# Optimization experiments

Hardware: AMD Instinct MI355X
Metric: run time of the kernel (lower is better)

## Reference

```python
import jax, jax.numpy as jnp
import numpy as np

N, D = 16384, 32            # nodes, max neighbors (0-padded)
INP, U = 256, 128           # input_units, units
R, ENT = 8, 8               # relations, entity types (relation/entity id 0 = padding for relations)


def setup_inputs() -> dict:
    key = jax.random.key(0)
    ks = jax.random.split(key, 12)
    s = 0.05  # scale learned params for numerical sanity (torch init is raw randn)
    return {
        "node_state": jax.random.normal(ks[0], (N, INP), dtype=jnp.float32),
        "adjacency": jax.random.randint(ks[1], (N, D), 0, N + 1, dtype=jnp.int32),  # 0 = pad row
        "point_enc": jax.random.randint(ks[2], (N,), 0, ENT, dtype=jnp.int32),
        "relation_enc": jax.random.randint(ks[3], (N, D), 0, R, dtype=jnp.int32),   # 0 = pad edge
        "point_enc_w": jax.random.normal(ks[4], (ENT, INP, U), dtype=jnp.float32) * s,
        "relation_enc_w": jax.random.normal(ks[5], (R, U, U), dtype=jnp.float32) * s,
        "q_w": jax.random.normal(ks[6], (U, U), dtype=jnp.float32) * s,
        "k_w": jax.random.normal(ks[7], (U, U), dtype=jnp.float32) * s,
        "v_w": jax.random.normal(ks[8], (U, U), dtype=jnp.float32) * s,
        "fc_w": jax.random.normal(ks[9], (U, U), dtype=jnp.float32) * s,
        "fc_b": jax.random.normal(ks[10], (U,), dtype=jnp.float32) * s,
    }


def reference(node_state, adjacency, point_enc, relation_enc,
              point_enc_w, relation_enc_w, q_w, k_w, v_w, fc_w, fc_b):
    ent, inp, u = point_enc_w.shape
    r_cnt = relation_enc_w.shape[0]
    dt = node_state.dtype

    # center = node_state @ point_enc_w[point_enc]; loop over small fixed entity set
    # to avoid materializing an (N, INP, U) gathered weight tensor.
    center = jnp.zeros((node_state.shape[0], u), dtype=dt)
    for e in range(ent):
        center = center + jnp.where(point_enc[:, None] == e,
                                    node_state @ point_enc_w[e], 0.0)

    # prepend zero row: adjacency index 0 == padding neighbor
    padded = jnp.concatenate([jnp.zeros((1, u), dtype=dt), center], axis=0)  # (N+1, U)
    x = padded[adjacency]  # (N, D, U) gathered neighbor embeddings

    # neighbors = x @ relation_enc_w[relation_enc]; per-relation GEMM + mask
    # (same math as the per-edge gathered matmul, without the E*U*U blowup)
    neighbors = jnp.zeros_like(x)
    for r in range(r_cnt):
        neighbors = neighbors + jnp.where(relation_enc[..., None] == r,
                                          jnp.einsum('ndu,uv->ndv', x, relation_enc_w[r]), 0.0)

    scale = u ** 0.5
    q = (center @ q_w) / scale                               # (N, U)
    k = jnp.einsum('ndu,uv->ndv', neighbors, k_w) / scale    # (N, D, U)
    v = jnp.einsum('ndu,uv->ndv', neighbors, v_w)            # (N, D, U)

    scores = jnp.einsum('nu,ndu->nd', q, k)                  # (N, D)
    scores = jnp.where(relation_enc == 0, jnp.asarray(-1e9, dt), scores)
    attn = jax.nn.softmax(scores, axis=-1)                   # over neighbors
    agg = jnp.einsum('nd,ndu->nu', attn, v)                  # (N, U)

    return center + jax.nn.relu(agg @ fc_w + fc_b)           # (N, U)
```

## Files before the change

kernel.cpp:

```cpp
#include <hip/hip_runtime.h>

#define NNODE 16384
#define DD 32
#define INPC 256
#define UC 128
#define RC 8
#define EC 8

typedef __attribute__((ext_vector_type(8))) short short8;
typedef __attribute__((ext_vector_type(4))) float float4v;
typedef __attribute__((ext_vector_type(4))) unsigned uint4v;

__device__ __forceinline__ unsigned short f2bf(float f) {
    unsigned u = __builtin_bit_cast(unsigned, f);
    unsigned r = (u + 0x7FFFu + ((u >> 16) & 1u)) >> 16;
    return (unsigned short)r;
}
__device__ __forceinline__ float bf2f(unsigned short s) { return __builtin_bit_cast(float, (unsigned)s << 16); }

template <int CTRL>
__device__ __forceinline__ float dppq(float x) {
    return __builtin_bit_cast(float,
        __builtin_amdgcn_mov_dpp(__builtin_bit_cast(int, x), CTRL, 0xF, 0xF, true));
}
#define DPP_XOR1 0xB1
#define DPP_XOR2 0x4E

__device__ __forceinline__ short8 ld8bf(const float* p) {
    float4 v0 = *(const float4*)p;
    float4 v1 = *(const float4*)(p + 4);
    short8 a;
    a[0] = (short)f2bf(v0.x); a[1] = (short)f2bf(v0.y);
    a[2] = (short)f2bf(v0.z); a[3] = (short)f2bf(v0.w);
    a[4] = (short)f2bf(v1.x); a[5] = (short)f2bf(v1.y);
    a[6] = (short)f2bf(v1.z); a[7] = (short)f2bf(v1.w);
    return a;
}

__device__ __forceinline__ int bfrag_idx(int k, int col, int nct) {
    int ks = k >> 5, ct = col >> 4;
    int l = (((k >> 3) & 3) << 4) | (col & 15);
    return (((ks * nct + ct) << 6) + l) * 8 + (k & 7);
}

__global__ void k_setup(const float* __restrict__ pew, const float* __restrict__ qw,
                        const float* __restrict__ kw, const float* __restrict__ relw,
                        const float* __restrict__ vw, const float* __restrict__ fcw,
                        unsigned short* __restrict__ pewfrag,
                        unsigned short* __restrict__ BallQfrag, unsigned short* __restrict__ RVFfrag) {
    __shared__ unsigned short stage_s[128 * 132];
    __shared__ unsigned short mat_s[16 * 136];
    int b = blockIdx.x;
    if (b < 256) {
        #pragma unroll
        for (int it = 0; it < 4; ++it) {
            int id = it * 65536 + b * 256 + threadIdx.x;
            int e = id >> 15, k = (id >> 7) & 255, col = id & 127;
            pewfrag[(e << 15) + bfrag_idx(k, col, 8)] = f2bf(pew[id]);
        }
        return;
    }
    {
        int pb = b - 256;
        int r = pb & 7, i0 = (pb >> 3) * 16;
        int w = threadIdx.x >> 6, l = threadIdx.x & 63;
        int mrow = l & 15, kgrp = (l >> 4) << 3;
        const float* R = relw + r * (UC * UC);

        float4v accP[2] = {};
        #pragma unroll
        for (int ks = 0; ks < 4; ++ks) {
            short8 a = ld8bf(&qw[(i0 + mrow) * UC + ks * 32 + kgrp]);
            #pragma unroll
            for (int ci = 0; ci < 2; ++ci) {
                int ct = w * 2 + ci;
                short8 bf = ld8bf(&kw[(ct * 16 + mrow) * UC + ks * 32 + kgrp]);
                accP[ci] = __builtin_amdgcn_mfma_f32_16x16x32_bf16(a, bf, accP[ci], 0, 0, 0);
            }
        }
        #pragma unroll
        for (int ci = 0; ci < 2; ++ci)
            #pragma unroll
            for (int reg = 0; reg < 4; ++reg) {
                int row = ((l >> 4) << 2) + reg;
                int col = (w * 2 + ci) * 16 + mrow;
                mat_s[row * 136 + col] = f2bf(accP[ci][reg] * (1.0f / 128.0f));
            }
        for (int it = 0; it < 16; ++it) {
            int idx = it * 256 + threadIdx.x;
            int row = idx >> 5, col = (idx & 31) * 4;
            float4 v = *(const float4*)&vw[row * UC + col];
            uint2 o;
            o.x = (unsigned)f2bf(v.x) | ((unsigned)f2bf(v.y) << 16);
            o.y = (unsigned)f2bf(v.z) | ((unsigned)f2bf(v.w) << 16);
            *(uint2*)&stage_s[row * 132 + col] = o;
        }
        __syncthreads();

        float4v accM[2] = {}, accV[2] = {};
        #pragma unroll
        for (int ks = 0; ks < 4; ++ks) {
            short8 aM = *(const short8*)&mat_s[mrow * 136 + ks * 32 + kgrp];
            short8 aV = ld8bf(&R[(i0 + mrow) * UC + ks * 32 + kgrp]);
            #pragma unroll
            for (int ci = 0; ci < 2; ++ci) {
                int ct = w * 2 + ci;
                short8 bM = ld8bf(&R[(ct * 16 + mrow) * UC + ks * 32 + kgrp]);
                accM[ci] = __builtin_amdgcn_mfma_f32_16x16x32_bf16(aM, bM, accM[ci], 0, 0, 0);
                uint4v pv;
                #pragma unroll
                for (int jp = 0; jp < 4; ++jp) {
                    unsigned e0 = stage_s[(ks * 32 + kgrp + jp * 2) * 132 + ct * 16 + mrow];
                    unsigned e1 = stage_s[(ks * 32 + kgrp + jp * 2 + 1) * 132 + ct * 16 + mrow];
                    pv[jp] = e0 | (e1 << 16);
                }
                accV[ci] = __builtin_amdgcn_mfma_f32_16x16x32_bf16(
                    aV, __builtin_bit_cast(short8, pv), accV[ci], 0, 0, 0);
            }
        }
        #pragma unroll
        for (int ci = 0; ci < 2; ++ci)
            #pragma unroll
            for (int reg = 0; reg < 4; ++reg) {
                int i = i0 + ((l >> 4) << 2) + reg;
                int col = r * 128 + (w * 2 + ci) * 16 + mrow;
                BallQfrag[bfrag_idx(i, col, 64)] = f2bf(accM[ci][reg]);
            }
        __syncthreads();
        #pragma unroll
        for (int ci = 0; ci < 2; ++ci)
            #pragma unroll
            for (int reg = 0; reg < 4; ++reg)
                mat_s[(((l >> 4) << 2) + reg) * 136 + (w * 2 + ci) * 16 + mrow] = f2bf(accV[ci][reg]);
        for (int it = 0; it < 16; ++it) {
            int idx = it * 256 + threadIdx.x;
            int row = idx >> 5, col = (idx & 31) * 4;
            float4 v = *(const float4*)&fcw[row * UC + col];
            uint2 o;
            o.x = (unsigned)f2bf(v.x) | ((unsigned)f2bf(v.y) << 16);
            o.y = (unsigned)f2bf(v.z) | ((unsigned)f2bf(v.w) << 16);
            *(uint2*)&stage_s[row * 132 + col] = o;
        }
        __syncthreads();

        float4v accF[2] = {};
        #pragma unroll
        for (int ks = 0; ks < 4; ++ks) {
            short8 aF = *(const short8*)&mat_s[mrow * 136 + ks * 32 + kgrp];
            #pragma unroll
            for (int ci = 0; ci < 2; ++ci) {
                int ct = w * 2 + ci;
                uint4v pv;
                #pragma unroll
                for (int jp = 0; jp < 4; ++jp) {
                    unsigned e0 = stage_s[(ks * 32 + kgrp + jp * 2) * 132 + ct * 16 + mrow];
                    unsigned e1 = stage_s[(ks * 32 + kgrp + jp * 2 + 1) * 132 + ct * 16 + mrow];
                    pv[jp] = e0 | (e1 << 16);
                }
                accF[ci] = __builtin_amdgcn_mfma_f32_16x16x32_bf16(
                    aF, __builtin_bit_cast(short8, pv), accF[ci], 0, 0, 0);
            }
        }
        #pragma unroll
        for (int ci = 0; ci < 2; ++ci)
            #pragma unroll
            for (int reg = 0; reg < 4; ++reg) {
                int i = i0 + ((l >> 4) << 2) + reg;
                int col = (w * 2 + ci) * 16 + mrow;
                RVFfrag[bfrag_idx(r * 128 + i, col, 8)] = f2bf(accF[ci][reg]);
            }
    }
}

__global__ __launch_bounds__(256, 4)
void k_center(const float* __restrict__ ns, const unsigned short* __restrict__ pewfrag,
              const int* __restrict__ pe, unsigned short* __restrict__ center_bf) {
    int w = threadIdx.x >> 6, l = threadIdx.x & 63;
    int n0 = blockIdx.x * 16;
    int row = n0 + (l & 15);
    int ent = pe[row];

    short8 a[8];
    #pragma unroll
    for (int ks = 0; ks < 8; ++ks)
        a[ks] = ld8bf(&ns[(size_t)row * 256 + ks * 32 + ((l >> 4) << 3)]);

    float4v acc[2] = {};
    short8 z = {};
    for (int e = 0; e < 8; ++e) {
        if (!__any(ent == e)) continue;
        const unsigned short* pf = pewfrag + ((size_t)e << 15);
        #pragma unroll
        for (int ks = 0; ks < 8; ++ks) {
            short8 am = (ent == e) ? a[ks] : z;
            #pragma unroll
            for (int ci = 0; ci < 2; ++ci) {
                int ct = w * 2 + ci;
                short8 b = *(const short8*)&pf[(((ks * 8 + ct) << 6) + l) * 8];
                acc[ci] = __builtin_amdgcn_mfma_f32_16x16x32_bf16(am, b, acc[ci], 0, 0, 0);
            }
        }
    }
    #pragma unroll
    for (int reg = 0; reg < 4; ++reg) {
        int orow = n0 + ((l >> 4) << 2) + reg;
        #pragma unroll
        for (int ci = 0; ci < 2; ++ci)
            center_bf[(size_t)orow * 128 + (w * 2 + ci) * 16 + (l & 15)] = f2bf(acc[ci][reg]);
    }
}

#define QSTRIDE 1096
__global__ __launch_bounds__(256, 4)
void k_final(const unsigned short* __restrict__ center_bf,
             const unsigned short* __restrict__ BallQfrag,
             const unsigned short* __restrict__ RVFfrag,
             const int* __restrict__ adj, const int* __restrict__ rel,
             const float* __restrict__ fcb, float* __restrict__ out) {
    __shared__ unsigned short qlds[16 * QSTRIDE];
    int w = threadIdx.x >> 6, l = threadIdx.x & 63;
    int n0 = blockIdx.x * 16;

    int pk[4][2];
    #pragma unroll
    for (int q = 0; q < 4; ++q) {
        int n = n0 + w * 4 + q;
        #pragma unroll
        for (int t = 0; t < 2; ++t) {
            int ai = adj[n * DD + t * 16 + (l & 15)];
            int rv = rel[n * DD + t * 16 + (l & 15)];
            int rr = ai > 0 ? ai - 1 : 0;
            pk[q][t] = (rr << 5) | (rv << 1) | (ai != 0 ? 1 : 0);
        }
    }

    short8 xp[2][4];
    #pragma unroll
    for (int t = 0; t < 2; ++t)
        #pragma unroll
        for (int ks = 0; ks < 4; ++ks)
            xp[t][ks] = *(const short8*)&center_bf[(size_t)(pk[0][t] >> 5) * 128
                                                   + ks * 32 + ((l >> 4) << 3)];

    {
        short8 a[4];
        #pragma unroll
        for (int ks = 0; ks < 4; ++ks)
            a[ks] = *(const short8*)&center_bf[(size_t)(n0 + (l & 15)) * 128 + ks * 32 + ((l >> 4) << 3)];
        for (int ci = 0; ci < 16; ++ci) {
            int ct = w * 16 + ci;
            float4v acc = {};
            #pragma unroll
            for (int ks = 0; ks < 4; ++ks) {
                short8 b = *(const short8*)&BallQfrag[(((ks * 64 + ct) << 6) + l) * 8];
                acc = __builtin_amdgcn_mfma_f32_16x16x32_bf16(a[ks], b, acc, 0, 0, 0);
            }
            int r = ct >> 3;
            int ch = (ct & 7) * 16 + (l & 15);
            #pragma unroll
            for (int reg = 0; reg < 4; ++reg) {
                int rn = ((l >> 4) << 2) + reg;
                qlds[rn * QSTRIDE + r * 136 + ch] = f2bf(acc[reg]);
            }
        }
    }
    __syncthreads();

    #pragma unroll
    for (int q = 0; q < 4; ++q) {
        int tn = w * 4 + q;
        int p0 = pk[q][0], p1 = pk[q][1];
        int rv0 = (p0 >> 1) & 7, rv1 = (p1 >> 1) & 7;
        int va0 = p0 & 1, va1 = p1 & 1;

        float4v sc[2] = {};
        #pragma unroll
        for (int ks = 0; ks < 4; ++ks) {
            short8 qb = *(const short8*)&qlds[tn * QSTRIDE + (l & 7) * 136 + ks * 32 + ((l >> 4) << 3)];
            sc[0] = __builtin_amdgcn_mfma_f32_16x16x32_bf16(qb, xp[0][ks], sc[0], 0, 0, 0);
            sc[1] = __builtin_amdgcn_mfma_f32_16x16x32_bf16(qb, xp[1][ks], sc[1], 0, 0, 0);
        }

        int rsel = (l & 32) ? (p1 >> 5) : (p0 >> 5);
        int rows[8];
        #pragma unroll
        for (int jj = 0; jj < 8; ++jj)
            rows[jj] = __shfl(rsel, (l & 48) | (((l >> 4) & 1) * 8 + jj), 64);
        unsigned short g0[4][8];
        #pragma unroll
        for (int ct = 0; ct < 4; ++ct)
            #pragma unroll
            for (int jj = 0; jj < 8; ++jj)
                g0[ct][jj] = center_bf[(size_t)rows[jj] * 128 + ct * 16 + (l & 15)];

        if (q < 3) {
            #pragma unroll
            for (int t = 0; t < 2; ++t)
                #pragma unroll
                for (int ks = 0; ks < 4; ++ks)
                    xp[t][ks] = *(const short8*)&center_bf[(size_t)(pk[q + 1][t] >> 5) * 128
                                                           + ks * 32 + ((l >> 4) << 3)];
        }

        float sel0, sel1;
        {
            int r = rv0;
            float v01 = (r & 1) ? sc[0][1] : sc[0][0];
            float v23 = (r & 1) ? sc[0][3] : sc[0][2];
            float regv = (r & 2) ? v23 : v01;
            float s = __shfl(regv, ((r >> 2) << 4) | (l & 15), 64);
            if (!va0) s = 0.f;
            if (r == 0) s = -1e9f;
            sel0 = fminf(s, 60.f);
        }
        {
            int r = rv1;
            float v01 = (r & 1) ? sc[1][1] : sc[1][0];
            float v23 = (r & 1) ? sc[1][3] : sc[1][2];
            float regv = (r & 2) ? v23 : v01;
            float s = __shfl(regv, ((r >> 2) << 4) | (l & 15), 64);
            if (!va1) s = 0.f;
            if (r == 0) s = -1e9f;
            sel1 = fminf(s, 60.f);
        }

        float at0 = __expf(sel0);
        float at1 = __expf(sel1);
        float sm = at0 + at1;
        sm += dppq<DPP_XOR1>(sm);
        sm += dppq<DPP_XOR2>(sm);
        sm += __shfl_xor(sm, 4, 64);
        sm += __shfl_xor(sm, 8, 64);
        float inv = 1.0f / fmaxf(sm, 1e-30f);
        at0 *= inv; at1 *= inv;
        if (!va0) at0 = 0.f;
        if (!va1) at1 = 0.f;

        unsigned md0 = (unsigned)f2bf(at0) | ((unsigned)rv0 << 16);
        unsigned md1 = (unsigned)f2bf(at1) | ((unsigned)rv1 << 16);
        unsigned mdsel = (l >= 32) ? md1 : md0;
        unsigned aw[4];
        #pragma unroll
        for (int jp = 0; jp < 4; ++jp) {
            unsigned m0 = __shfl(mdsel, (l & 48) | (((l >> 4) & 1) * 8 + jp * 2), 64);
            unsigned m1 = __shfl(mdsel, (l & 48) | (((l >> 4) & 1) * 8 + jp * 2 + 1), 64);
            unsigned s0 = ((m0 >> 16) == (unsigned)(l & 15)) ? (m0 & 0xFFFFu) : 0u;
            unsigned s1 = ((m1 >> 16) == (unsigned)(l & 15)) ? (m1 & 0xFFFFu) : 0u;
            aw[jp] = s0 | (s1 << 16);
        }
        uint4v av = {aw[0], aw[1], aw[2], aw[3]};
        short8 afrag = __builtin_bit_cast(short8, av);

        #pragma unroll
        for (int ct = 0; ct < 4; ++ct) {
            uint4v bv = {(unsigned)g0[ct][0] | ((unsigned)g0[ct][1] << 16),
                         (unsigned)g0[ct][2] | ((unsigned)g0[ct][3] << 16),
                         (unsigned)g0[ct][4] | ((unsigned)g0[ct][5] << 16),
                         (unsigned)g0[ct][6] | ((unsigned)g0[ct][7] << 16)};
            float4v zc = {};
            float4v acc = __builtin_amdgcn_mfma_f32_16x16x32_bf16(
                afrag, __builtin_bit_cast(short8, bv), zc, 0, 0, 0);
            if (l < 32) {
                int rbase = (l >> 4) << 2;
                #pragma unroll
                for (int reg = 0; reg < 4; ++reg)
                    qlds[tn * QSTRIDE + (rbase + reg) * 136 + ct * 16 + (l & 15)] = f2bf(acc[reg]);
            }
        }

        unsigned short g1[4][8];
        #pragma unroll
        for (int c2 = 0; c2 < 4; ++c2)
            #pragma unroll
            for (int jj = 0; jj < 8; ++jj)
                g1[c2][jj] = center_bf[(size_t)rows[jj] * 128 + (c2 + 4) * 16 + (l & 15)];
        #pragma unroll
        for (int c2 = 0; c2 < 4; ++c2) {
            int ct = c2 + 4;
            uint4v bv = {(unsigned)g1[c2][0] | ((unsigned)g1[c2][1] << 16),
                         (unsigned)g1[c2][2] | ((unsigned)g1[c2][3] << 16),
                         (unsigned)g1[c2][4] | ((unsigned)g1[c2][5] << 16),
                         (unsigned)g1[c2][6] | ((unsigned)g1[c2][7] << 16)};
            float4v zc = {};
            float4v acc = __builtin_amdgcn_mfma_f32_16x16x32_bf16(
                afrag, __builtin_bit_cast(short8, bv), zc, 0, 0, 0);
            if (l < 32) {
                int rbase = (l >> 4) << 2;
                #pragma unroll
                for (int reg = 0; reg < 4; ++reg)
                    qlds[tn * QSTRIDE + (rbase + reg) * 136 + ct * 16 + (l & 15)] = f2bf(acc[reg]);
            }
        }
    }
    __syncthreads();

    {
        float4v acc[2] = {};
        #pragma unroll 4
        for (int ks = 0; ks < 32; ++ks) {
            short8 a = *(const short8*)&qlds[(l & 15) * QSTRIDE + (ks >> 2) * 136
                                             + (ks & 3) * 32 + ((l >> 4) << 3)];
            #pragma unroll
            for (int ci = 0; ci < 2; ++ci) {
                int ct = w * 2 + ci;
                short8 b = *(const short8*)&RVFfrag[(((ks * 8 + ct) << 6) + l) * 8];
                acc[ci] = __builtin_amdgcn_mfma_f32_16x16x32_bf16(a, b, acc[ci], 0, 0, 0);
            }
        }
        #pragma unroll
        for (int ci = 0; ci < 2; ++ci) {
            int ct = w * 2 + ci;
            int col = ct * 16 + (l & 15);
            float bb = fcb[col];
            #pragma unroll
            for (int reg = 0; reg < 4; ++reg) {
                int n = n0 + ((l >> 4) << 2) + reg;
                float v = acc[ci][reg] + bb;
                v = v > 0.f ? v : 0.f;
                out[(size_t)n * 128 + col] = bf2f(center_bf[(size_t)n * 128 + col]) + v;
            }
        }
    }
}

extern "C" void kernel_launch(void* const* d_in, const int* in_sizes, int n_in,
                              void* d_out, int out_size, void* d_ws, size_t ws_size,
                              hipStream_t stream) {
    const float* node_state = (const float*)d_in[0];
    const int*   adjacency  = (const int*)d_in[1];
    const int*   point_enc  = (const int*)d_in[2];
    const int*   relation   = (const int*)d_in[3];
    const float* pew        = (const float*)d_in[4];
    const float* relw       = (const float*)d_in[5];
    const float* qw         = (const float*)d_in[6];
    const float* kw         = (const float*)d_in[7];
    const float* vw         = (const float*)d_in[8];
    const float* fcw        = (const float*)d_in[9];
    const float* fcb        = (const float*)d_in[10];
    float* out = (float*)d_out;

    char* ws = (char*)d_ws;
    unsigned short* BallQfrag = (unsigned short*)ws;  ws += 128 * 1024 * 2;
    unsigned short* RVFfrag   = (unsigned short*)ws;  ws += 1024 * 128 * 2;
    unsigned short* center_bf = (unsigned short*)ws;  ws += (size_t)NNODE * 128 * 2;
    unsigned short* pewfrag   = (unsigned short*)ws;  ws += 8 * 32768 * 2;

    k_setup<<<320, 256, 0, stream>>>(pew, qw, kw, relw, vw, fcw,
                                     pewfrag, BallQfrag, RVFfrag);
    k_center<<<NNODE / 16, 256, 0, stream>>>(node_state, pewfrag, point_enc, center_bf);
    k_final<<<NNODE / 16, 256, 0, stream>>>(center_bf, BallQfrag, RVFfrag,
                                            adjacency, relation, fcb, out);
}
```

Measured before the change: 163.7 us.

## Tile k_center over 64 rows with LDS-staged activations to reuse weight fragments

k_center now processes 64 nodes per block instead of 16. The node_state rows are staged as bf16 in shared memory, and each weight fragment loaded from global memory is reused across four 16-row tiles. This cuts repeated per-entity weight loads, which matters because with random entity ids nearly every tile touches all 8 entities. In exchange the kernel uses more LDS and accumulator registers and launches a quarter as many blocks, which may reduce occupancy.

```diff
diff --git a/kernel.cpp b/kernel.cpp
--- a/kernel.cpp
+++ b/kernel.cpp
@@ -175,39 +175,68 @@
 __global__ __launch_bounds__(256, 4)
 void k_center(const float* __restrict__ ns, const unsigned short* __restrict__ pewfrag,
               const int* __restrict__ pe, unsigned short* __restrict__ center_bf) {
+    __shared__ unsigned short asmem[64][264];
     int w = threadIdx.x >> 6, l = threadIdx.x & 63;
-    int n0 = blockIdx.x * 16;
-    int row = n0 + (l & 15);
-    int ent = pe[row];
-
-    short8 a[8];
+    int n0 = blockIdx.x * 64;
+
+    for (int it = 0; it < 8; ++it) {
+        int c = it * 256 + threadIdx.x;
+        int row = c >> 5, ch0 = (c & 31) << 3;
+        *(short8*)&asmem[row][ch0] = ld8bf(&ns[(size_t)(n0 + row) * 256 + ch0]);
+    }
+    int ent0 = pe[n0 + 0 * 16 + (l & 15)];
+    int ent1 = pe[n0 + 1 * 16 + (l & 15)];
+    int ent2 = pe[n0 + 2 * 16 + (l & 15)];
+    int ent3 = pe[n0 + 3 * 16 + (l & 15)];
+    __syncthreads();
+
+    float4v acc[4][2] = {};
+    short8 z = {};
     #pragma unroll
-    for (int ks = 0; ks < 8; ++ks)
-        a[ks] = ld8bf(&ns[(size_t)row * 256 + ks * 32 + ((l >> 4) << 3)]);
-
-    float4v acc[2] = {};
-    short8 z = {};
     for (int e = 0; e < 8; ++e) {
-        if (!__any(ent == e)) continue;
+        bool p0 = __any(ent0 == e), p1 = __any(ent1 == e);
+        bool p2 = __any(ent2 == e), p3 = __any(ent3 == e);
+        if (!(p0 | p1 | p2 | p3)) continue;
         const unsigned short* pf = pewfrag + ((size_t)e << 15);
         #pragma unroll
         for (int ks = 0; ks < 8; ++ks) {
-            short8 am = (ent == e) ? a[ks] : z;
-            #pragma unroll
-            for (int ci = 0; ci < 2; ++ci) {
-                int ct = w * 2 + ci;
-                short8 b = *(const short8*)&pf[(((ks * 8 + ct) << 6) + l) * 8];
-                acc[ci] = __builtin_amdgcn_mfma_f32_16x16x32_bf16(am, b, acc[ci], 0, 0, 0);
+            short8 b0 = *(const short8*)&pf[(((ks * 8 + w * 2 + 0) << 6) + l) * 8];
+            short8 b1 = *(const short8*)&pf[(((ks * 8 + w * 2 + 1) << 6) + l) * 8];
+            if (p0) {
+                short8 a = *(const short8*)&asmem[0 * 16 + (l & 15)][ks * 32 + ((l >> 4) << 3)];
+                short8 am = (ent0 == e) ? a : z;
+                acc[0][0] = __builtin_amdgcn_mfma_f32_16x16x32_bf16(am, b0, acc[0][0], 0, 0, 0);
+                acc[0][1] = __builtin_amdgcn_mfma_f32_16x16x32_bf16(am, b1, acc[0][1], 0, 0, 0);
+            }
+            if (p1) {
+                short8 a = *(const short8*)&asmem[1 * 16 + (l & 15)][ks * 32 + ((l >> 4) << 3)];
+                short8 am = (ent1 == e) ? a : z;
+                acc[1][0] = __builtin_amdgcn_mfma_f32_16x16x32_bf16(am, b0, acc[1][0], 0, 0, 0);
+                acc[1][1] = __builtin_amdgcn_mfma_f32_16x16x32_bf16(am, b1, acc[1][1], 0, 0, 0);
+            }
+            if (p2) {
+                short8 a = *(const short8*)&asmem[2 * 16 + (l & 15)][ks * 32 + ((l >> 4) << 3)];
+                short8 am = (ent2 == e) ? a : z;
+                acc[2][0] = __builtin_amdgcn_mfma_f32_16x16x32_bf16(am, b0, acc[2][0], 0, 0, 0);
+                acc[2][1] = __builtin_amdgcn_mfma_f32_16x16x32_bf16(am, b1, acc[2][1], 0, 0, 0);
+            }
+            if (p3) {
+                short8 a = *(const short8*)&asmem[3 * 16 + (l & 15)][ks * 32 + ((l >> 4) << 3)];
+                short8 am = (ent3 == e) ? a : z;
+                acc[3][0] = __builtin_amdgcn_mfma_f32_16x16x32_bf16(am, b0, acc[3][0], 0, 0, 0);
+                acc[3][1] = __builtin_amdgcn_mfma_f32_16x16x32_bf16(am, b1, acc[3][1], 0, 0, 0);
             }
         }
     }
     #pragma unroll
-    for (int reg = 0; reg < 4; ++reg) {
-        int orow = n0 + ((l >> 4) << 2) + reg;
-        #pragma unroll
-        for (int ci = 0; ci < 2; ++ci)
-            center_bf[(size_t)orow * 128 + (w * 2 + ci) * 16 + (l & 15)] = f2bf(acc[ci][reg]);
-    }
+    for (int t = 0; t < 4; ++t)
+        #pragma unroll
+        for (int reg = 0; reg < 4; ++reg) {
+            int orow = n0 + t * 16 + ((l >> 4) << 2) + reg;
+            #pragma unroll
+            for (int ci = 0; ci < 2; ++ci)
+                center_bf[(size_t)orow * 128 + (w * 2 + ci) * 16 + (l & 15)] = f2bf(acc[t][ci][reg]);
+        }
 }
 
 #define QSTRIDE 1096
@@ -447,7 +476,7 @@
 
     k_setup<<<320, 256, 0, stream>>>(pew, qw, kw, relw, vw, fcw,
                                      pewfrag, BallQfrag, RVFfrag);
-    k_center<<<NNODE / 16, 256, 0, stream>>>(node_state, pewfrag, point_enc, center_bf);
+    k_center<<<NNODE / 64, 256, 0, stream>>>(node_state, pewfrag, point_enc, center_bf);
     k_final<<<NNODE / 16, 256, 0, stream>>>(center_bf, BallQfrag, RVFfrag,
                                             adjacency, relation, fcb, out);
 }
```

Result: no change. 166.9 us (+2.0%).
